# Kernel tuning notes

Hardware: AMD Instinct MI355X
Metric: run time of the kernel (lower is better)

Reference implementation:

```python
import jax, jax.numpy as jnp
import numpy as np

B, N, C = 2, 50000, 81          # images, proposals/image, classes (incl. background)
H, W = 800.0, 1333.0            # image shape
SCORE_THRESH = 0.05
NMS_THRESH = 0.5
DETS = 100                      # detections_per_img
K = 2048                        # pre-NMS candidates kept per image (padded)
BBOX_CLIP = 4.135166556742356   # log(1000/16), torchvision BoxCoder clamp
WX, WY, WW, WH = 10.0, 10.0, 5.0, 5.0  # bbox_reg_weights
MIN_SIZE = 0.01                 # remove_small_boxes threshold
LBL_OFFSET = 1401.0             # MAX_SIZE + 1, batched_nms class-offset trick


def setup_inputs() -> dict:
    key = jax.random.key(0)
    k1, k2, k3, k4 = jax.random.split(key, 4)
    class_logits = jax.random.normal(k1, (B * N, C), jnp.float32) * 2.0
    box_regression = jax.random.normal(k2, (B * N, C * 4), jnp.float32) * 0.5
    wh_img = jnp.array([W, H], jnp.float32)
    cxy = jax.random.uniform(k3, (B, N, 2), jnp.float32) * wh_img
    wh = jax.random.uniform(k4, (B, N, 2), jnp.float32) * 200.0 + 4.0
    x1y1 = jnp.clip(cxy - 0.5 * wh, 0.0, wh_img)
    x2y2 = jnp.clip(cxy + 0.5 * wh, 0.0, wh_img)
    proposals = jnp.concatenate([x1y1, x2y2], axis=-1)  # [B, N, 4] xyxy
    return {"class_logits": class_logits, "box_regression": box_regression, "proposals": proposals}


def _decode(rel, boxes):
    # rel [N, C, 4], boxes [N, 4] xyxy -> decoded [N, C, 4] (torchvision BoxCoder.decode)
    w = boxes[:, 2] - boxes[:, 0]
    h = boxes[:, 3] - boxes[:, 1]
    cx = boxes[:, 0] + 0.5 * w
    cy = boxes[:, 1] + 0.5 * h
    dx = rel[..., 0] / WX
    dy = rel[..., 1] / WY
    dw = jnp.minimum(rel[..., 2] / WW, BBOX_CLIP)
    dh = jnp.minimum(rel[..., 3] / WH, BBOX_CLIP)
    pcx = dx * w[:, None] + cx[:, None]
    pcy = dy * h[:, None] + cy[:, None]
    pw = jnp.exp(dw) * w[:, None]
    ph = jnp.exp(dh) * h[:, None]
    return jnp.stack([pcx - 0.5 * pw, pcy - 0.5 * ph, pcx + 0.5 * pw, pcy + 0.5 * ph], axis=-1)


def _pairwise_iou(a):
    # a [K, 4] -> [K, K]
    area = (a[:, 2] - a[:, 0]) * (a[:, 3] - a[:, 1])
    lt = jnp.maximum(a[:, None, :2], a[None, :, :2])
    rb = jnp.minimum(a[:, None, 2:], a[None, :, 2:])
    wh = jnp.clip(rb - lt, 0.0)
    inter = wh[..., 0] * wh[..., 1]
    return inter / (area[:, None] + area[None, :] - inter + 1e-9)


def _nms_keep(iou, valid):
    # sequential greedy NMS over score-sorted candidates
    Kn = iou.shape[0]
    def body(keep, i):
        sup = jnp.any(keep & (iou[i] > NMS_THRESH))
        keep = keep.at[i].set(valid[i] & ~sup)
        return keep, None
    keep, _ = jax.lax.scan(body, jnp.zeros((Kn,), bool), jnp.arange(Kn))
    return keep


def _per_image(logits, reg, props):
    # logits [N, C], reg [N, C*4], props [N, 4]
    scores = jax.nn.softmax(logits, axis=-1)[:, 1:]                  # drop background
    boxes = _decode(reg.reshape(N, C, 4), props)[:, 1:]              # [N, C-1, 4]
    boxes = jnp.stack([jnp.clip(boxes[..., 0], 0.0, W),
                       jnp.clip(boxes[..., 1], 0.0, H),
                       jnp.clip(boxes[..., 2], 0.0, W),
                       jnp.clip(boxes[..., 3], 0.0, H)], axis=-1)
    fb = boxes.reshape(-1, 4)                                        # [N*(C-1), 4]
    fs = scores.reshape(-1)
    fl = jnp.broadcast_to(jnp.arange(1, C), (N, C - 1)).reshape(-1)
    ws = fb[:, 2] - fb[:, 0]
    hs = fb[:, 3] - fb[:, 1]
    valid = (fs > SCORE_THRESH) & (ws >= MIN_SIZE) & (hs >= MIN_SIZE)
    masked = jnp.where(valid, fs, -1.0)
    top_s, top_i = jax.lax.top_k(masked, K)                          # sorted desc
    cb = fb[top_i]
    cl = fl[top_i]
    cvalid = top_s > 0.0
    # batched NMS: offset boxes by class so different classes never overlap
    ob = cb + cl.astype(cb.dtype)[:, None] * LBL_OFFSET
    keep = _nms_keep(_pairwise_iou(ob), cvalid)
    kept_s = jnp.where(keep, top_s, -1.0)
    out_s, sel = jax.lax.top_k(kept_s, DETS)
    m = out_s > 0.0
    out_b = cb[sel] * m[:, None].astype(cb.dtype)
    out_l = jnp.where(m, cl[sel], -1)
    return out_b, jnp.where(m, out_s, 0.0), out_l


def reference(class_logits, box_regression, proposals):
    logits = class_logits.reshape(B, N, C)
    reg = box_regression.reshape(B, N, C * 4)
    boxes, scores, labels = jax.vmap(_per_image)(logits, reg, proposals)
    return boxes, scores, labels  # [B, DETS, 4], [B, DETS], [B, DETS] (padded, score==0 invalid)
```

## Files before the change

### kernel.cpp

```cpp
#include <hip/hip_runtime.h>
#include <hip/hip_bf16.h>
#include <stdint.h>

#define Bn 2
#define Np 50000
#define Cc 81
#define CM1 80
#define KSEL 2048
#define NDET 100
#define NBUCK 2048
#define BUCK_BASE 0x3D000000u
#define BUCK_SHIFT 15
#define SELCAP 4096
#define IMG_W 1333.0f
#define IMG_H 800.0f
#define SCORE_TH 0.05f
#define MIN_SZ 0.01f
#define NMS_TH 0.5f
#define LBLOFF 1401.0f
#define BBOX_CLIP_F 4.135166556742356f
#define CHUNK 16
#define QCAP 320
#define BLKX 782
#define WPI  (BLKX*4)
#define RS_WPB 4

typedef unsigned long long u64;
typedef unsigned int u32;

__device__ __forceinline__ u64 shfl64(u64 v, int src) {
  int lo = __shfl((int)(u32)v, src, 64);
  int hi = __shfl((int)(u32)(v >> 32), src, 64);
  return ((u64)(u32)hi << 32) | (u32)lo;
}

__device__ __forceinline__ void decode_box(int row, int c,
    const float* __restrict__ reg, const float* __restrict__ props,
    float& x1, float& y1, float& x2, float& y2) {
  const float4 pr = *reinterpret_cast<const float4*>(props + (size_t)row * 4);
  float w = __fsub_rn(pr.z, pr.x), h = __fsub_rn(pr.w, pr.y);
  float cx = __fadd_rn(pr.x, 0.5f * w), cy = __fadd_rn(pr.y, 0.5f * h);
  const float4 rel = *reinterpret_cast<const float4*>(reg + ((size_t)row * Cc + c) * 4);
  float dx = __fdiv_rn(rel.x, 10.f), dy = __fdiv_rn(rel.y, 10.f);
  float dw = fminf(__fdiv_rn(rel.z, 5.f), BBOX_CLIP_F);
  float dh = fminf(__fdiv_rn(rel.w, 5.f), BBOX_CLIP_F);
  float pcx = __fadd_rn(__fmul_rn(dx, w), cx);
  float pcy = __fadd_rn(__fmul_rn(dy, h), cy);
  float pw = __fmul_rn(expf(dw), w);
  float ph = __fmul_rn(expf(dh), h);
  x1 = fminf(fmaxf(__fsub_rn(pcx, 0.5f * pw), 0.f), IMG_W);
  y1 = fminf(fmaxf(__fsub_rn(pcy, 0.5f * ph), 0.f), IMG_H);
  x2 = fminf(fmaxf(__fadd_rn(pcx, 0.5f * pw), 0.f), IMG_W);
  y2 = fminf(fmaxf(__fadd_rn(pcy, 0.5f * ph), 0.f), IMG_H);
}

__device__ __forceinline__ void decode_key_to_sel(u64 key, int b,
    const float* __restrict__ reg, const float* __restrict__ props,
    float* __restrict__ S, u32 pos) {
  const u32 sb = (u32)(key >> 32);
  const u32 idx = ~(u32)key;
  const int n_ = (int)(idx / CM1);
  const int c = (int)(idx % CM1) + 1;
  float x1, y1, x2, y2;
  decode_box(b * Np + n_, c, reg, props, x1, y1, x2, y2);
  S[0 * SELCAP + pos] = x1; S[1 * SELCAP + pos] = y1;
  S[2 * SELCAP + pos] = x2; S[3 * SELCAP + pos] = y2;
  S[4 * SELCAP + pos] = __uint_as_float(sb);
  S[5 * SELCAP + pos] = (float)c;
}

#define SOFTMAX_PROLOG(S)                                            \
  const int p = lane >> 2, qd = lane & 3;                            \
  const int base = p * Cc + qd * 21;                                 \
  const int cnt_k = (qd == 3) ? 18 : 21;                             \
  float ev[21];                                                      \
  _Pragma("unroll")                                                  \
  for (int k = 0; k < 21; ++k)                                       \
    ev[k] = (k < cnt_k) ? (S)[base + k] : -3.4e38f;                  \
  float m = ev[0];                                                   \
  _Pragma("unroll")                                                  \
  for (int k = 1; k < 21; ++k) m = fmaxf(m, ev[k]);                  \
  m = fmaxf(m, __shfl_xor(m, 1, 64));                                \
  m = fmaxf(m, __shfl_xor(m, 2, 64));                                \
  float s = 0.f;                                                     \
  _Pragma("unroll")                                                  \
  for (int k = 0; k < 21; ++k) {                                     \
    ev[k] = (k < cnt_k) ? expf(ev[k] - m) : 0.f;                     \
    s += ev[k];                                                      \
  }                                                                  \
  s += __shfl_xor(s, 1, 64);                                         \
  s += __shfl_xor(s, 2, 64);                                         \
  const float thr = SCORE_TH * s;

#define STAGE_LOGITS(S, src)                                         \
  _Pragma("unroll")                                                  \
  for (int i = 0; i < 6; ++i) {                                      \
    const int f4 = i * 64 + lane;                                    \
    if (f4 < (CHUNK * Cc) / 4) {                                     \
      const float4 v = *reinterpret_cast<const float4*>((src) + (size_t)f4 * 4); \
      *reinterpret_cast<float4*>(&(S)[f4 * 4]) = v;                  \
    }                                                                \
  }

__global__ __launch_bounds__(256, 4) void passA_kernel(
    const float* __restrict__ logits, u64* __restrict__ wseg,
    u32* __restrict__ wcnt, u32* __restrict__ ghist)
{
  __shared__ __align__(16) float stg[4][CHUNK * Cc];
  __shared__ u32 hist[NBUCK];
  const int b = blockIdx.y;
  const int tid = threadIdx.x;
  const int wave = tid >> 6, lane = tid & 63;
  for (int i = tid; i < NBUCK; i += 256) hist[i] = 0;
  __syncthreads();

  const int wslot = (blockIdx.x << 2) + wave;
  const int n0 = wslot * CHUNK;
  u64* seg = wseg + (size_t)(b * WPI + wslot) * QCAP;
  u32 wout = 0;
  if (n0 < Np) {
    float* S = stg[wave];
    STAGE_LOGITS(S, logits + ((size_t)b * Np + n0) * Cc)
    SOFTMAX_PROLOG(S)
    const int n_ = n0 + p;
    #pragma unroll
    for (int k = 0; k < 21; ++k) {
      const int c = qd * 21 + k;
      bool emit = false;
      u64 key = 0; u32 bk = 0;
      if (c > 0 && ev[k] > thr) {
        const u32 sb = __float_as_uint(__fdiv_rn(ev[k], s));
        const u32 idx = (u32)(n_ * CM1 + (c - 1));
        key = ((u64)sb << 32) | (u32)(~idx);
        bk = (sb - BUCK_BASE) >> BUCK_SHIFT;
        if (bk > (u32)(NBUCK - 1)) bk = NBUCK - 1;
        emit = true;
      }
      const u64 bal = __ballot(emit);
      if (emit) {
        seg[wout + (u32)__popcll(bal & ((1ull << lane) - 1ull))] = key;
        atomicAdd(&hist[bk], 1u);
      }
      wout += (u32)__popcll(bal);
    }
  }
  if (lane == 0) wcnt[b * WPI + wslot] = wout;
  __syncthreads();
  for (int i = tid; i < NBUCK; i += 256) {
    const u32 v = hist[i];
    if (v) atomicAdd(&ghist[b * NBUCK + i], v);
  }
}

__global__ void thresh_kernel(const u32* __restrict__ ghist, u32* __restrict__ gT,
                              u32* __restrict__ gTot, u32* __restrict__ boffs) {
  const int b = blockIdx.x;
  const int lane = threadIdx.x;
  const u32* h = ghist + b * NBUCK;
  u32* bo = boffs + b * NBUCK;
  const int SEG = NBUCK / 64;
  u32 segsum = 0;
  for (int t = 0; t < SEG; ++t) segsum += h[lane * SEG + t];
  u32 suf = segsum;
  #pragma unroll
  for (int o = 1; o < 64; o <<= 1) {
    const u32 v = (u32)__shfl_down((int)suf, o, 64);
    if (lane + o < 64) suf += v;
  }
  u32 acc = suf - segsum;
  int myT = -1; u32 totv = 0;
  for (int t = SEG - 1; t >= 0; --t) {
    const int bk = lane * SEG + t;
    bo[bk] = acc;
    acc += h[bk];
    if (myT < 0 && acc >= (u32)KSEL) { myT = bk; totv = acc; }
  }
  int Tg = myT;
  #pragma unroll
  for (int o = 32; o; o >>= 1) Tg = max(Tg, __shfl_xor(Tg, o, 64));
  if (Tg < 0) {
    if (lane == 0) { gT[b] = 0u; gTot[b] = (acc < (u32)SELCAP) ? acc : (u32)SELCAP; }
  } else if (myT == Tg) {
    gT[b] = (u32)Tg;
    gTot[b] = (totv < (u32)SELCAP) ? totv : (u32)SELCAP;
  }
}

__global__ __launch_bounds__(256) void scatter_kernel(
    const u64* __restrict__ wseg, const u32* __restrict__ wcnt,
    const u32* __restrict__ gT, const u32* __restrict__ boffs,
    u32* __restrict__ bfill, u64* __restrict__ skeys,
    const float* __restrict__ reg, const float* __restrict__ props)
{
  const int b = blockIdx.y;
  const u32 T = gT[b];
  const int wave = threadIdx.x >> 6, lane = threadIdx.x & 63;
  const u32 sgi = blockIdx.x * 4 + wave;
  if (sgi >= (u32)WPI) return;
  const u32 cnt = wcnt[b * WPI + sgi];
  const u64* seg = wseg + (size_t)(b * WPI + sgi) * QCAP;
  for (u32 i = lane; i < cnt; i += 64) {
    const u64 key = seg[i];
    const u32 sb = (u32)(key >> 32);
    u32 bk = (sb - BUCK_BASE) >> BUCK_SHIFT;
    if (bk > (u32)(NBUCK - 1)) bk = NBUCK - 1;
    if (bk >= T) {
      const u32 idx = ~(u32)key;
      const int pn = (int)(idx / CM1);
      const int c = (int)(idx % CM1) + 1;
      float x1, y1, x2, y2;
      decode_box(b * Np + pn, c, reg, props, x1, y1, x2, y2);
      if (__fsub_rn(x2, x1) >= MIN_SZ && __fsub_rn(y2, y1) >= MIN_SZ) {
        const u32 pos = boffs[b * NBUCK + bk] + atomicAdd(&bfill[b * NBUCK + bk], 1u);
        if (pos < (u32)SELCAP) skeys[(size_t)b * SELCAP + pos] = key;
      }
    }
  }
}

__global__ __launch_bounds__(256) void runsort_kernel(
    const u64* __restrict__ skeys, const u32* __restrict__ gT,
    const u32* __restrict__ boffs, const u32* __restrict__ bfill,
    const u32* __restrict__ ghist,
    const float* __restrict__ reg, const float* __restrict__ props,
    float* __restrict__ sel)
{
  const int b = blockIdx.y;
  const int wave = threadIdx.x >> 6, lane = threadIdx.x & 63;
  const u32 bk = blockIdx.x * RS_WPB + wave;
  if (bk >= (u32)NBUCK || bk < gT[b]) return;
  const u32 start = boffs[b * NBUCK + bk];
  if (start >= (u32)SELCAP) return;
  u32 Lp = bfill[b * NBUCK + bk];
  u32 Lh = ghist[b * NBUCK + bk];
  if (start + Lp > (u32)SELCAP) Lp = SELCAP - start;
  if (start + Lh > (u32)SELCAP) Lh = SELCAP - start;
  float* S = sel + (size_t)b * 6 * SELCAP;
  for (u32 j = Lp + lane; j < Lh; j += 64) S[4 * SELCAP + start + j] = 0.f;
  if (Lp == 0) return;
  const u64* run = skeys + (size_t)b * SELCAP + start;
  if (Lp <= 128u) {
    const u64 k0 = (lane < (int)Lp) ? run[lane] : 0ull;
    const u64 k1 = (64 + lane < (int)Lp) ? run[64 + lane] : 0ull;
    u32 r0 = 0, r1 = 0;
    #pragma unroll
    for (int l = 0; l < 64; ++l) {
      const u64 o0 = shfl64(k0, l);
      const u64 o1 = shfl64(k1, l);
      r0 += (o0 > k0) + (o1 > k0);
      r1 += (o0 > k1) + (o1 > k1);
    }
    if (lane < (int)Lp) decode_key_to_sel(k0, b, reg, props, S, start + r0);
    if (64 + lane < (int)Lp) decode_key_to_sel(k1, b, reg, props, S, start + r1);
  } else {
    for (u32 i = lane; i < Lp; i += 64) {
      const u64 k = run[i];
      u32 r = 0;
      for (u32 q = 0; q < Lp; ++q) r += (run[q] > k);
      decode_key_to_sel(k, b, reg, props, S, start + r);
    }
  }
}

__global__ __launch_bounds__(64) void tail_kernel(
    const float* __restrict__ sel, const u32* __restrict__ gTot,
    float* __restrict__ out)
{
  __shared__ float kox1[NDET], koy1[NDET], kox2[NDET], koy2[NDET], kar[NDET];
  __shared__ float kx1[NDET], ky1[NDET], kx2[NDET], ky2[NDET], ksc[NDET], klb[NDET];
  const int b = blockIdx.x;
  const int lane = threadIdx.x;
  const u32 total = gTot[b];
  const float* S = sel + (size_t)b * 6 * SELCAP;
  int kc = 0;
  for (u32 bbase = 0; bbase < total && kc < NDET; bbase += 64) {
    const u32 pos = bbase + lane;
    const bool inb = pos < total;
    float x1 = 0, y1 = 0, x2 = 0, y2 = 0, sc = 0, lb = 0;
    if (inb) {
      x1 = S[0 * SELCAP + pos]; y1 = S[1 * SELCAP + pos];
      x2 = S[2 * SELCAP + pos]; y2 = S[3 * SELCAP + pos];
      sc = S[4 * SELCAP + pos]; lb = S[5 * SELCAP + pos];
    }
    const float offv = __fmul_rn(lb, LBLOFF);
    const float ox1 = __fadd_rn(x1, offv), oy1 = __fadd_rn(y1, offv);
    const float ox2 = __fadd_rn(x2, offv), oy2 = __fadd_rn(y2, offv);
    const float ar = __fmul_rn(__fsub_rn(ox2, ox1), __fsub_rn(oy2, oy1));
    const bool valid = inb && (sc > 0.f);
    bool sup = false;
    for (int k = 0; k < kc; ++k) {
      const float ltx = fmaxf(ox1, kox1[k]), lty = fmaxf(oy1, koy1[k]);
      const float rbx = fminf(ox2, kox2[k]), rby = fminf(oy2, koy2[k]);
      const float wx = fmaxf(__fsub_rn(rbx, ltx), 0.f);
      const float wy = fmaxf(__fsub_rn(rby, lty), 0.f);
      const float inter = __fmul_rn(wx, wy);
      const float denom = __fadd_rn(__fsub_rn(__fadd_rn(ar, kar[k]), inter), 1e-9f);
      if (__fdiv_rn(inter, denom) > NMS_TH) sup = true;
    }
    u64 rem = __ballot(sup) | ~__ballot(valid);
    u64 todo = ~rem;
    while (todo && kc < NDET) {
      const int jb = (int)__builtin_ctzll(todo);
      const float bx1 = __shfl(ox1, jb, 64), by1 = __shfl(oy1, jb, 64);
      const float bx2 = __shfl(ox2, jb, 64), by2 = __shfl(oy2, jb, 64);
      const float ba  = __shfl(ar, jb, 64);
      if (lane == jb) {
        kox1[kc] = ox1; koy1[kc] = oy1; kox2[kc] = ox2; koy2[kc] = oy2; kar[kc] = ar;
        kx1[kc] = x1; ky1[kc] = y1; kx2[kc] = x2; ky2[kc] = y2; ksc[kc] = sc; klb[kc] = lb;
      }
      const float ltx = fmaxf(ox1, bx1), lty = fmaxf(oy1, by1);
      const float rbx = fminf(ox2, bx2), rby = fminf(oy2, by2);
      const float wx = fmaxf(__fsub_rn(rbx, ltx), 0.f);
      const float wy = fmaxf(__fsub_rn(rby, lty), 0.f);
      const float inter = __fmul_rn(wx, wy);
      const float denom = __fadd_rn(__fsub_rn(__fadd_rn(ar, ba), inter), 1e-9f);
      const u64 w = __ballot(__fdiv_rn(inter, denom) > NMS_TH);
      rem |= w;
      todo &= ~rem;
      todo &= ~(1ull << jb);
      ++kc;
    }
  }
  const int kcl = (kc < NDET) ? kc : NDET;
  for (int k = lane; k < NDET; k += 64) {
    float bx1 = 0, by1 = 0, bx2 = 0, by2 = 0, sc = 0, lb = -1.f;
    if (k < kcl) {
      bx1 = kx1[k]; by1 = ky1[k]; bx2 = kx2[k]; by2 = ky2[k];
      sc = ksc[k]; lb = klb[k];
    }
    float* ob = out + (size_t)b * NDET * 4;
    ob[k * 4 + 0] = bx1; ob[k * 4 + 1] = by1;
    ob[k * 4 + 2] = bx2; ob[k * 4 + 3] = by2;
    out[Bn * NDET * 4 + b * NDET + k] = sc;
    out[Bn * NDET * 4 + Bn * NDET + b * NDET + k] = lb;
  }
}

extern "C" void kernel_launch(void* const* d_in, const int* in_sizes, int n_in,
                              void* d_out, int out_size, void* d_ws, size_t ws_size,
                              hipStream_t stream) {
  const float* logits = (const float*)d_in[0];
  const float* reg    = (const float*)d_in[1];
  const float* props  = (const float*)d_in[2];
  float* out = (float*)d_out;
  char* ws = (char*)d_ws;

  u32* gT   = (u32*)ws;
  u32* gTot = (u32*)(ws + 16);
  size_t off = 64;
  u32* ghist = (u32*)(ws + off); off += (size_t)Bn * NBUCK * 4;
  u32* bfill = (u32*)(ws + off); off += (size_t)Bn * NBUCK * 4;
  const size_t memset_bytes = off;
  u32* boffs = (u32*)(ws + off); off += (size_t)Bn * NBUCK * 4;
  u64* skeys = (u64*)(ws + off); off += (size_t)Bn * SELCAP * 8;
  float* sel = (float*)(ws + off); off += (size_t)Bn * 6 * SELCAP * 4;
  u32* wcnt  = (u32*)(ws + off); off += (size_t)Bn * WPI * 4;
  off = (off + 255) & ~(size_t)255;
  u64* wseg  = (u64*)(ws + off); off += (size_t)Bn * WPI * QCAP * 8;
  (void)ws_size;

  hipMemsetAsync(d_ws, 0, memset_bytes, stream);
  passA_kernel<<<dim3(BLKX, Bn), 256, 0, stream>>>(logits, wseg, wcnt, ghist);
  thresh_kernel<<<dim3(Bn), 64, 0, stream>>>(ghist, gT, gTot, boffs);
  scatter_kernel<<<dim3((WPI + 3) / 4, Bn), 256, 0, stream>>>(wseg, wcnt, gT, boffs, bfill, skeys, reg, props);
  runsort_kernel<<<dim3(NBUCK / RS_WPB, Bn), 256, 0, stream>>>(skeys, gT, boffs, bfill, ghist, reg, props, sel);
  tail_kernel<<<dim3(Bn), 64, 0, stream>>>(sel, gTot, out);
}
```

Measured before the change: 89.98 us.

## Fuse per-bucket sort into tail NMS kernel with lazy batched decode

Removes the separate runsort kernel and the sel buffer. The tail kernel, now 256 threads, loads the bucketed keys into shared memory, sorts buckets lazily in batches of 512 positions, and decodes boxes only for batches NMS actually reaches, stopping early once 100 detections are kept. Pass A also replaces the per-class ballot compaction with one wave prefix scan of per-lane emit counts. This trades a kernel launch and global round trips for serial work in only 2 blocks, and the skeys region is now zeroed so padding slots read as empty keys.

```diff
diff --git a/kernel.cpp b/kernel.cpp
--- a/kernel.cpp
+++ b/kernel.cpp
@@ -11,6 +11,7 @@
 #define NBUCK 2048
 #define BUCK_BASE 0x3D000000u
 #define BUCK_SHIFT 15
+#define BUCK_MAX 1280
 #define SELCAP 4096
 #define IMG_W 1333.0f
 #define IMG_H 800.0f
@@ -23,16 +24,10 @@
 #define QCAP 320
 #define BLKX 782
 #define WPI  (BLKX*4)
-#define RS_WPB 4
+#define BATCH 512
 
 typedef unsigned long long u64;
 typedef unsigned int u32;
-
-__device__ __forceinline__ u64 shfl64(u64 v, int src) {
-  int lo = __shfl((int)(u32)v, src, 64);
-  int hi = __shfl((int)(u32)(v >> 32), src, 64);
-  return ((u64)(u32)hi << 32) | (u32)lo;
-}
 
 __device__ __forceinline__ void decode_box(int row, int c,
     const float* __restrict__ reg, const float* __restrict__ props,
@@ -52,21 +47,6 @@
   y1 = fminf(fmaxf(__fsub_rn(pcy, 0.5f * ph), 0.f), IMG_H);
   x2 = fminf(fmaxf(__fadd_rn(pcx, 0.5f * pw), 0.f), IMG_W);
   y2 = fminf(fmaxf(__fadd_rn(pcy, 0.5f * ph), 0.f), IMG_H);
-}
-
-__device__ __forceinline__ void decode_key_to_sel(u64 key, int b,
-    const float* __restrict__ reg, const float* __restrict__ props,
-    float* __restrict__ S, u32 pos) {
-  const u32 sb = (u32)(key >> 32);
-  const u32 idx = ~(u32)key;
-  const int n_ = (int)(idx / CM1);
-  const int c = (int)(idx % CM1) + 1;
-  float x1, y1, x2, y2;
-  decode_box(b * Np + n_, c, reg, props, x1, y1, x2, y2);
-  S[0 * SELCAP + pos] = x1; S[1 * SELCAP + pos] = y1;
-  S[2 * SELCAP + pos] = x2; S[3 * SELCAP + pos] = y2;
-  S[4 * SELCAP + pos] = __uint_as_float(sb);
-  S[5 * SELCAP + pos] = (float)c;
 }
 
 #define SOFTMAX_PROLOG(S)                                            \
@@ -117,34 +97,41 @@
   const int wslot = (blockIdx.x << 2) + wave;
   const int n0 = wslot * CHUNK;
   u64* seg = wseg + (size_t)(b * WPI + wslot) * QCAP;
-  u32 wout = 0;
+  u32 wtot = 0;
   if (n0 < Np) {
     float* S = stg[wave];
     STAGE_LOGITS(S, logits + ((size_t)b * Np + n0) * Cc)
     SOFTMAX_PROLOG(S)
     const int n_ = n0 + p;
+    u32 emask = 0;
     #pragma unroll
     for (int k = 0; k < 21; ++k) {
       const int c = qd * 21 + k;
-      bool emit = false;
-      u64 key = 0; u32 bk = 0;
-      if (c > 0 && ev[k] > thr) {
+      if (c > 0 && ev[k] > thr) emask |= (1u << k);
+    }
+    const u32 mycnt = __popc(emask);
+    u32 inc = mycnt;
+    #pragma unroll
+    for (int o = 1; o < 64; o <<= 1) {
+      const u32 v = (u32)__shfl_up((int)inc, o, 64);
+      if (lane >= o) inc += v;
+    }
+    u32 pos = inc - mycnt;
+    wtot = (u32)__shfl((int)inc, 63, 64);
+    #pragma unroll
+    for (int k = 0; k < 21; ++k) {
+      if (emask & (1u << k)) {
+        const int c = qd * 21 + k;
         const u32 sb = __float_as_uint(__fdiv_rn(ev[k], s));
         const u32 idx = (u32)(n_ * CM1 + (c - 1));
-        key = ((u64)sb << 32) | (u32)(~idx);
-        bk = (sb - BUCK_BASE) >> BUCK_SHIFT;
+        seg[pos++] = ((u64)sb << 32) | (u32)(~idx);
+        u32 bk = (sb - BUCK_BASE) >> BUCK_SHIFT;
         if (bk > (u32)(NBUCK - 1)) bk = NBUCK - 1;
-        emit = true;
-      }
-      const u64 bal = __ballot(emit);
-      if (emit) {
-        seg[wout + (u32)__popcll(bal & ((1ull << lane) - 1ull))] = key;
         atomicAdd(&hist[bk], 1u);
       }
-      wout += (u32)__popcll(bal);
-    }
-  }
-  if (lane == 0) wcnt[b * WPI + wslot] = wout;
+    }
+  }
+  if (lane == 0) wcnt[b * WPI + wslot] = wtot;
   __syncthreads();
   for (int i = tid; i < NBUCK; i += 256) {
     const u32 v = hist[i];
@@ -218,121 +205,173 @@
   }
 }
 
-__global__ __launch_bounds__(256) void runsort_kernel(
+__global__ __launch_bounds__(256) void tail_kernel(
     const u64* __restrict__ skeys, const u32* __restrict__ gT,
-    const u32* __restrict__ boffs, const u32* __restrict__ bfill,
-    const u32* __restrict__ ghist,
+    const u32* __restrict__ gTot, const u32* __restrict__ boffs,
     const float* __restrict__ reg, const float* __restrict__ props,
-    float* __restrict__ sel)
-{
-  const int b = blockIdx.y;
-  const int wave = threadIdx.x >> 6, lane = threadIdx.x & 63;
-  const u32 bk = blockIdx.x * RS_WPB + wave;
-  if (bk >= (u32)NBUCK || bk < gT[b]) return;
-  const u32 start = boffs[b * NBUCK + bk];
-  if (start >= (u32)SELCAP) return;
-  u32 Lp = bfill[b * NBUCK + bk];
-  u32 Lh = ghist[b * NBUCK + bk];
-  if (start + Lp > (u32)SELCAP) Lp = SELCAP - start;
-  if (start + Lh > (u32)SELCAP) Lh = SELCAP - start;
-  float* S = sel + (size_t)b * 6 * SELCAP;
-  for (u32 j = Lp + lane; j < Lh; j += 64) S[4 * SELCAP + start + j] = 0.f;
-  if (Lp == 0) return;
-  const u64* run = skeys + (size_t)b * SELCAP + start;
-  if (Lp <= 128u) {
-    const u64 k0 = (lane < (int)Lp) ? run[lane] : 0ull;
-    const u64 k1 = (64 + lane < (int)Lp) ? run[64 + lane] : 0ull;
-    u32 r0 = 0, r1 = 0;
-    #pragma unroll
-    for (int l = 0; l < 64; ++l) {
-      const u64 o0 = shfl64(k0, l);
-      const u64 o1 = shfl64(k1, l);
-      r0 += (o0 > k0) + (o1 > k0);
-      r1 += (o0 > k1) + (o1 > k1);
-    }
-    if (lane < (int)Lp) decode_key_to_sel(k0, b, reg, props, S, start + r0);
-    if (64 + lane < (int)Lp) decode_key_to_sel(k1, b, reg, props, S, start + r1);
-  } else {
-    for (u32 i = lane; i < Lp; i += 64) {
-      const u64 k = run[i];
-      u32 r = 0;
-      for (u32 q = 0; q < Lp; ++q) r += (run[q] > k);
-      decode_key_to_sel(k, b, reg, props, S, start + r);
-    }
-  }
-}
-
-__global__ __launch_bounds__(64) void tail_kernel(
-    const float* __restrict__ sel, const u32* __restrict__ gTot,
     float* __restrict__ out)
 {
+  __shared__ u64 skl[SELCAP];
+  __shared__ u32 sbo[NBUCK];
+  __shared__ float sx1[BATCH], sy1[BATCH], sx2[BATCH], sy2[BATCH];
+  __shared__ float ssc[BATCH], slb[BATCH];
+  __shared__ u32 lsrc[BATCH], lwid[BATCH];
   __shared__ float kox1[NDET], koy1[NDET], kox2[NDET], koy2[NDET], kar[NDET];
   __shared__ float kx1[NDET], ky1[NDET], kx2[NDET], ky2[NDET], ksc[NDET], klb[NDET];
+  __shared__ u32 sh_ns, sh_wend, sh_kc; __shared__ int sh_bk;
   const int b = blockIdx.x;
-  const int lane = threadIdx.x;
-  const u32 total = gTot[b];
-  const float* S = sel + (size_t)b * 6 * SELCAP;
+  const int tid = threadIdx.x;
+  const int wave = tid >> 6, lane = tid & 63;
+  const u32 T = gT[b];
+  const u32 gTotb = gTot[b];
+  const u32 TOT = (gTotb < (u32)KSEL) ? gTotb : (u32)KSEL;
+  for (int i = tid; i < SELCAP; i += 256) skl[i] = skeys[(size_t)b * SELCAP + i];
+  for (int i = tid; i < NBUCK; i += 256) sbo[i] = boffs[b * NBUCK + i];
+  if (tid == 0) { sh_kc = 0; sh_bk = BUCK_MAX; }
+  __syncthreads();
+
+  u32 wbeg = 0;
   int kc = 0;
-  for (u32 bbase = 0; bbase < total && kc < NDET; bbase += 64) {
-    const u32 pos = bbase + lane;
-    const bool inb = pos < total;
-    float x1 = 0, y1 = 0, x2 = 0, y2 = 0, sc = 0, lb = 0;
-    if (inb) {
-      x1 = S[0 * SELCAP + pos]; y1 = S[1 * SELCAP + pos];
-      x2 = S[2 * SELCAP + pos]; y2 = S[3 * SELCAP + pos];
-      sc = S[4 * SELCAP + pos]; lb = S[5 * SELCAP + pos];
-    }
-    const float offv = __fmul_rn(lb, LBLOFF);
-    const float ox1 = __fadd_rn(x1, offv), oy1 = __fadd_rn(y1, offv);
-    const float ox2 = __fadd_rn(x2, offv), oy2 = __fadd_rn(y2, offv);
-    const float ar = __fmul_rn(__fsub_rn(ox2, ox1), __fsub_rn(oy2, oy1));
-    const bool valid = inb && (sc > 0.f);
-    bool sup = false;
-    for (int k = 0; k < kc; ++k) {
-      const float ltx = fmaxf(ox1, kox1[k]), lty = fmaxf(oy1, koy1[k]);
-      const float rbx = fminf(ox2, kox2[k]), rby = fminf(oy2, koy2[k]);
-      const float wx = fmaxf(__fsub_rn(rbx, ltx), 0.f);
-      const float wy = fmaxf(__fsub_rn(rby, lty), 0.f);
-      const float inter = __fmul_rn(wx, wy);
-      const float denom = __fadd_rn(__fsub_rn(__fadd_rn(ar, kar[k]), inter), 1e-9f);
-      if (__fdiv_rn(inter, denom) > NMS_TH) sup = true;
-    }
-    u64 rem = __ballot(sup) | ~__ballot(valid);
-    u64 todo = ~rem;
-    while (todo && kc < NDET) {
-      const int jb = (int)__builtin_ctzll(todo);
-      const float bx1 = __shfl(ox1, jb, 64), by1 = __shfl(oy1, jb, 64);
-      const float bx2 = __shfl(ox2, jb, 64), by2 = __shfl(oy2, jb, 64);
-      const float ba  = __shfl(ar, jb, 64);
-      if (lane == jb) {
-        kox1[kc] = ox1; koy1[kc] = oy1; kox2[kc] = ox2; koy2[kc] = oy2; kar[kc] = ar;
-        kx1[kc] = x1; ky1[kc] = y1; kx2[kc] = x2; ky2[kc] = y2; ksc[kc] = sc; klb[kc] = lb;
-      }
-      const float ltx = fmaxf(ox1, bx1), lty = fmaxf(oy1, by1);
-      const float rbx = fminf(ox2, bx2), rby = fminf(oy2, by2);
-      const float wx = fmaxf(__fsub_rn(rbx, ltx), 0.f);
-      const float wy = fmaxf(__fsub_rn(rby, lty), 0.f);
-      const float inter = __fmul_rn(wx, wy);
-      const float denom = __fadd_rn(__fsub_rn(__fadd_rn(ar, ba), inter), 1e-9f);
-      const u64 w = __ballot(__fdiv_rn(inter, denom) > NMS_TH);
-      rem |= w;
-      todo &= ~rem;
-      todo &= ~(1ull << jb);
-      ++kc;
-    }
-  }
+  while (kc < NDET && wbeg < TOT) {
+    if (tid == 0) {
+      const u32 wend_t = (wbeg + (u32)BATCH < TOT) ? (wbeg + (u32)BATCH) : TOT;
+      int bk = sh_bk;
+      u32 ns = 0;
+      while (bk >= (int)T && sbo[bk] < wend_t && ns < (u32)BATCH) {
+        const u32 st = sbo[bk];
+        u32 nxt = (bk > 0) ? sbo[bk - 1] : gTotb;
+        if (nxt > gTotb) nxt = gTotb;
+        if (nxt > st) { lsrc[ns] = st; lwid[ns] = nxt - st; ++ns; }
+        --bk;
+      }
+      sh_ns = ns; sh_wend = wend_t; sh_bk = bk;
+    }
+    __syncthreads();
+    const u32 ns = sh_ns;
+    const u32 wend = sh_wend;
+    for (u32 e = wave; e < ns; e += 4) {
+      const u32 st = lsrc[e], W = lwid[e];
+      if (W < 2) continue;
+      if (W <= 128u) {
+        const u64 k0 = (lane < (int)W) ? skl[st + lane] : 0ull;
+        const u64 k1 = (64 + lane < (int)W) ? skl[st + 64 + lane] : 0ull;
+        u32 r0 = 0, r1 = 0;
+        for (u32 q = 0; q < W; ++q) {
+          const u64 kq = skl[st + q];
+          r0 += (kq > k0); r1 += (kq > k1);
+        }
+        if (lane < (int)W) skl[st + r0] = k0;
+        if (64 + lane < (int)W) skl[st + r1] = k1;
+      } else if (W <= 512u) {
+        u64 kk[8]; u32 rr[8];
+        #pragma unroll
+        for (int j = 0; j < 8; ++j) {
+          kk[j] = ((u32)(j * 64) + lane < W) ? skl[st + j * 64 + lane] : 0ull;
+          rr[j] = 0;
+        }
+        for (u32 q = 0; q < W; ++q) {
+          const u64 kq = skl[st + q];
+          #pragma unroll
+          for (int j = 0; j < 8; ++j) rr[j] += (kq > kk[j]);
+        }
+        #pragma unroll
+        for (int j = 0; j < 8; ++j)
+          if ((u32)(j * 64) + lane < W) skl[st + rr[j]] = kk[j];
+      } else {
+        for (u32 ph = 0; ph < W; ++ph)
+          for (u32 q = lane; 2 * q + (ph & 1) + 1 < W; q += 64) {
+            const u32 i0 = st + 2 * q + (ph & 1);
+            const u64 a = skl[i0], c2 = skl[i0 + 1];
+            if (a < c2) { skl[i0] = c2; skl[i0 + 1] = a; }
+          }
+      }
+    }
+    __syncthreads();
+    const u32 bn = wend - wbeg;
+    for (u32 i = tid; i < bn; i += 256) {
+      const u64 key = skl[wbeg + i];
+      float x1 = 0, y1 = 0, x2 = 0, y2 = 0, sc = 0, lb = 0;
+      if (key) {
+        const u32 sb = (u32)(key >> 32);
+        const u32 idx = ~(u32)key;
+        const int n_ = (int)(idx / CM1);
+        const int c = (int)(idx % CM1) + 1;
+        sc = __uint_as_float(sb);
+        decode_box(b * Np + n_, c, reg, props, x1, y1, x2, y2);
+        lb = (float)c;
+      }
+      sx1[i] = x1; sy1[i] = y1; sx2[i] = x2; sy2[i] = y2; ssc[i] = sc; slb[i] = lb;
+    }
+    __syncthreads();
+    if (wave == 0) {
+      int kcl = kc;
+      for (u32 base = 0; base < bn && kcl < NDET; base += 64) {
+        const u32 pos = base + lane;
+        const bool inb = pos < bn;
+        float x1 = 0, y1 = 0, x2 = 0, y2 = 0, sc = 0, lb = 0;
+        if (inb) {
+          x1 = sx1[pos]; y1 = sy1[pos]; x2 = sx2[pos]; y2 = sy2[pos];
+          sc = ssc[pos]; lb = slb[pos];
+        }
+        const float offv = __fmul_rn(lb, LBLOFF);
+        const float ox1 = __fadd_rn(x1, offv), oy1 = __fadd_rn(y1, offv);
+        const float ox2 = __fadd_rn(x2, offv), oy2 = __fadd_rn(y2, offv);
+        const float ar = __fmul_rn(__fsub_rn(ox2, ox1), __fsub_rn(oy2, oy1));
+        const bool valid = inb && (sc > 0.f);
+        bool sup = false;
+        for (int k = 0; k < kcl; ++k) {
+          const float ltx = fmaxf(ox1, kox1[k]), lty = fmaxf(oy1, koy1[k]);
+          const float rbx = fminf(ox2, kox2[k]), rby = fminf(oy2, koy2[k]);
+          const float wx = fmaxf(__fsub_rn(rbx, ltx), 0.f);
+          const float wy = fmaxf(__fsub_rn(rby, lty), 0.f);
+          const float inter = __fmul_rn(wx, wy);
+          const float denom = __fadd_rn(__fsub_rn(__fadd_rn(ar, kar[k]), inter), 1e-9f);
+          if (__fdiv_rn(inter, denom) > NMS_TH) sup = true;
+        }
+        u64 rem = __ballot(sup) | ~__ballot(valid);
+        u64 todo = ~rem;
+        while (todo && kcl < NDET) {
+          const int jb = (int)__builtin_ctzll(todo);
+          const float bx1 = __shfl(ox1, jb, 64), by1 = __shfl(oy1, jb, 64);
+          const float bx2 = __shfl(ox2, jb, 64), by2 = __shfl(oy2, jb, 64);
+          const float ba  = __shfl(ar, jb, 64);
+          if (lane == jb) {
+            kox1[kcl] = ox1; koy1[kcl] = oy1; kox2[kcl] = ox2; koy2[kcl] = oy2; kar[kcl] = ar;
+            kx1[kcl] = x1; ky1[kcl] = y1; kx2[kcl] = x2; ky2[kcl] = y2; ksc[kcl] = sc; klb[kcl] = lb;
+          }
+          const float ltx = fmaxf(ox1, bx1), lty = fmaxf(oy1, by1);
+          const float rbx = fminf(ox2, bx2), rby = fminf(oy2, by2);
+          const float wx = fmaxf(__fsub_rn(rbx, ltx), 0.f);
+          const float wy = fmaxf(__fsub_rn(rby, lty), 0.f);
+          const float inter = __fmul_rn(wx, wy);
+          const float denom = __fadd_rn(__fsub_rn(__fadd_rn(ar, ba), inter), 1e-9f);
+          const u64 w = __ballot(__fdiv_rn(inter, denom) > NMS_TH);
+          rem |= w;
+          todo &= ~rem;
+          todo &= ~(1ull << jb);
+          ++kcl;
+        }
+      }
+      if (lane == 0) sh_kc = (u32)kcl;
+    }
+    __syncthreads();
+    kc = (int)sh_kc;
+    wbeg = wend;
+  }
+
+  __syncthreads();
   const int kcl = (kc < NDET) ? kc : NDET;
-  for (int k = lane; k < NDET; k += 64) {
+  if (tid < NDET) {
     float bx1 = 0, by1 = 0, bx2 = 0, by2 = 0, sc = 0, lb = -1.f;
-    if (k < kcl) {
-      bx1 = kx1[k]; by1 = ky1[k]; bx2 = kx2[k]; by2 = ky2[k];
-      sc = ksc[k]; lb = klb[k];
+    if (tid < kcl) {
+      bx1 = kx1[tid]; by1 = ky1[tid]; bx2 = kx2[tid]; by2 = ky2[tid];
+      sc = ksc[tid]; lb = klb[tid];
     }
     float* ob = out + (size_t)b * NDET * 4;
-    ob[k * 4 + 0] = bx1; ob[k * 4 + 1] = by1;
-    ob[k * 4 + 2] = bx2; ob[k * 4 + 3] = by2;
-    out[Bn * NDET * 4 + b * NDET + k] = sc;
-    out[Bn * NDET * 4 + Bn * NDET + b * NDET + k] = lb;
+    ob[tid * 4 + 0] = bx1; ob[tid * 4 + 1] = by1;
+    ob[tid * 4 + 2] = bx2; ob[tid * 4 + 3] = by2;
+    out[Bn * NDET * 4 + b * NDET + tid] = sc;
+    out[Bn * NDET * 4 + Bn * NDET + b * NDET + tid] = lb;
   }
 }
 
@@ -350,10 +389,9 @@
   size_t off = 64;
   u32* ghist = (u32*)(ws + off); off += (size_t)Bn * NBUCK * 4;
   u32* bfill = (u32*)(ws + off); off += (size_t)Bn * NBUCK * 4;
+  u64* skeys = (u64*)(ws + off); off += (size_t)Bn * SELCAP * 8;
   const size_t memset_bytes = off;
   u32* boffs = (u32*)(ws + off); off += (size_t)Bn * NBUCK * 4;
-  u64* skeys = (u64*)(ws + off); off += (size_t)Bn * SELCAP * 8;
-  float* sel = (float*)(ws + off); off += (size_t)Bn * 6 * SELCAP * 4;
   u32* wcnt  = (u32*)(ws + off); off += (size_t)Bn * WPI * 4;
   off = (off + 255) & ~(size_t)255;
   u64* wseg  = (u64*)(ws + off); off += (size_t)Bn * WPI * QCAP * 8;
@@ -363,6 +401,5 @@
   passA_kernel<<<dim3(BLKX, Bn), 256, 0, stream>>>(logits, wseg, wcnt, ghist);
   thresh_kernel<<<dim3(Bn), 64, 0, stream>>>(ghist, gT, gTot, boffs);
   scatter_kernel<<<dim3((WPI + 3) / 4, Bn), 256, 0, stream>>>(wseg, wcnt, gT, boffs, bfill, skeys, reg, props);
-  runsort_kernel<<<dim3(NBUCK / RS_WPB, Bn), 256, 0, stream>>>(skeys, gT, boffs, bfill, ghist, reg, props, sel);
-  tail_kernel<<<dim3(Bn), 64, 0, stream>>>(sel, gTot, out);
-}
+  tail_kernel<<<dim3(Bn), 256, 0, stream>>>(skeys, gT, gTot, boffs, reg, props, out);
+}
```

Result: slower. 111.6 us (+24.0%).
